# Kernel tuning notes

Hardware: AMD Instinct MI355X
Metric: run time of the kernel (lower is better)

Reference implementation:

```python
import jax, jax.numpy as jnp
import numpy as np
import math

# Model config (see init_kwargs)
E = 1024   # emb_size
H = 8      # ffwd_num_head
D = 128    # ffwd_head_size (E == H*D)
NE = 16    # ffwd_num_expert
A = 2      # ffwd_num_expert_active
S = 256    # ffwd_expert_size
B = 2      # batch_size_fwd
T = 2048   # context_window
NUM_BLOCK = 12


def setup_inputs() -> dict:
    key = jax.random.key(0)
    ks = jax.random.split(key, 5)
    x = jax.random.normal(ks[0], (B, T, E), jnp.float32)
    # fc_in_fused: Linear(E, 4E+NE, bias=False), torch weight shape (out,in)
    w_in = 0.02 * jax.random.normal(ks[1], (4 * E + NE, E), jnp.float32)
    # fc_out_fused: Linear(2E, E), std 0.02/sqrt(num_block)
    w_out = (0.02 / math.sqrt(NUM_BLOCK)) * jax.random.normal(ks[2], (E, 2 * E), jnp.float32)
    # k_ffwd/v_ffwd: original (1,H,NE*S,D); stored here as (NE,H,S,D) for per-expert scan
    k_ffwd = 0.02 * jax.random.normal(ks[3], (NE, H, S, D), jnp.float32)
    v_ffwd = 0.02 * jax.random.normal(ks[4], (NE, H, S, D), jnp.float32)
    return {"x": x, "w_in": w_in, "w_out": w_out, "k_ffwd": k_ffwd, "v_ffwd": v_ffwd}


def _rope(t):
    # Standard half-split RoPE, base 10000. t: (B,T,H,D)
    half = t.shape[-1] // 2
    inv_freq = 1.0 / (10000.0 ** (jnp.arange(half, dtype=jnp.float32) / half))
    ang = jnp.arange(t.shape[1], dtype=jnp.float32)[:, None] * inv_freq  # (T, half)
    cos = jnp.cos(ang)[None, :, None, :]
    sin = jnp.sin(ang)[None, :, None, :]
    t1, t2 = t[..., :half], t[..., half:]
    return jnp.concatenate([t1 * cos - t2 * sin, t1 * sin + t2 * cos], axis=-1)


def reference(x, w_in, w_out, k_ffwd, v_ffwd):
    Bx, Tx, _ = x.shape
    h = x @ w_in.T  # (B,T,4E+NE)
    q_f, q_a, k_a, v_a, router_logits = jnp.split(h, [E, 2 * E, 3 * E, 4 * E], axis=-1)

    # top-k routing (order of the k slots is irrelevant: outputs are summed)
    gate_logits, assign = jax.lax.top_k(router_logits, A)  # (B,T,A)
    gate = jax.nn.sigmoid(gate_logits)

    # --- attention half: causal softmax attention, scale 1/sqrt(D), with RoPE ---
    q = _rope(q_a.reshape(Bx, Tx, H, D))
    k = _rope(k_a.reshape(Bx, Tx, H, D))
    v = v_a.reshape(Bx, Tx, H, D)
    scores = jnp.einsum('bqhd,bkhd->bhqk', q, k) / math.sqrt(D)
    causal = jnp.tril(jnp.ones((Tx, Tx), dtype=bool))
    scores = jnp.where(causal, scores, -jnp.inf)
    p = jax.nn.softmax(scores, axis=-1)
    attn_out = jnp.einsum('bhqk,bkhd->bqhd', p, v).reshape(Bx, Tx, E)

    # --- MoE-FFN half, expressed as attention with score_mod log1p(gelu):
    # exp(lse)*softmax recovers sum_s (1+gelu(q.k_s)) v_s; subtracting sum_s v_s
    # leaves sum_s gelu(q.k_s) v_s over the assigned expert's slots. ---
    qf = q_f.reshape(Bx, Tx, H, D)

    def step(acc, ekv):
        e, ke, ve = ekv  # ke, ve: (H,S,D)
        s = jnp.einsum('bthd,hsd->bths', qf, ke)
        a = jax.nn.gelu(s, approximate=False)  # torch F.gelu default = exact erf
        o = jnp.einsum('bths,hsd->bthd', a, ve)
        g = jnp.sum(jnp.where(assign == e, gate, 0.0), axis=-1)  # (B,T)
        return acc + g[..., None, None] * o, None

    acc0 = jnp.zeros((Bx, Tx, H, D), x.dtype)
    ffwd_out, _ = jax.lax.scan(step, acc0, (jnp.arange(NE), k_ffwd, v_ffwd))
    ffwd_out = ffwd_out.reshape(Bx, Tx, E)

    out = jnp.concatenate([attn_out, ffwd_out], axis=-1) @ w_out.T  # (B,T,E)
    return out
```

## Files before the change

kernel.cpp:

```cpp
#include <hip/hip_runtime.h>
#include <hip/hip_bf16.h>
#include <math.h>

#define E 1024
#define NHP 4096
#define NEXP 16
#define HH 8
#define DD 128
#define SS 256
#define BB 2
#define TT 2048
#define BT 4096

typedef __attribute__((ext_vector_type(8))) short bf16x8;
typedef __attribute__((ext_vector_type(4))) float f32x4;

#define GLDS16(g, s) __builtin_amdgcn_global_load_lds( \
    (const __attribute__((address_space(1))) void*)(g), \
    (__attribute__((address_space(3))) void*)(s), 16, 0, 0)

__device__ __forceinline__ ushort f2b(float f) {
    union { float f; unsigned u; } v; v.f = f;
    unsigned r = (v.u + 0x7FFFu + ((v.u >> 16) & 1u)) >> 16;
    return (ushort)r;
}
__device__ __forceinline__ float b2f(ushort u) {
    union { unsigned u; float f; } v; v.u = ((unsigned)u) << 16;
    return v.f;
}
__device__ __forceinline__ float gelu_fast(float x) {
    float u2 = x * x;
    float tu = x * (1.5957691216f + 0.0713548163f * u2);
    float e = __expf(tu);
    float sig = 1.f - __builtin_amdgcn_rcpf(e + 1.f);
    return x * sig;
}

__global__ void cvtk_swz(const float* __restrict__ in, ushort* __restrict__ outp,
                         int kshift, int n)
{
    int i = (blockIdx.x * blockDim.x + threadIdx.x) * 8;
    if (i >= n) return;
    int row = i >> kshift;
    int colb = (i - (row << kshift)) * 2;
    float4 f0 = *(const float4*)(in + i);
    float4 f1 = *(const float4*)(in + i + 4);
    ushort4 u0, u1;
    u0.x = f2b(f0.x); u0.y = f2b(f0.y); u0.z = f2b(f0.z); u0.w = f2b(f0.w);
    u1.x = f2b(f1.x); u1.y = f2b(f1.y); u1.z = f2b(f1.z); u1.w = f2b(f1.w);
    char* dst = (char*)outp + ((size_t)row << (kshift + 1)) + (colb ^ ((row & 7) << 4));
    *(ushort4*)dst = u0;
    *(ushort4*)(dst + 8) = u1;
}

template<int BF16OUT>
__global__ __launch_bounds__(256) void gemm_bf16(
    const ushort* __restrict__ A, int lda,
    const ushort* __restrict__ B, int ldb,
    void* __restrict__ Cv, int ldc, int K)
{
    __shared__ ushort As[128 * 64];
    __shared__ ushort Bs[128 * 64];
    const int t = threadIdx.x;
    const int l = t & 63, w = t >> 6;
    const int m0 = blockIdx.y * 128, n0 = blockIdx.x * 128;
    const int wr = w >> 1, wc = w & 1;
    const int fr = l & 15, fg = l >> 4;

    const int srow = w * 32 + (l >> 3);
    const int sboff = (l & 7) * 16;
    const char* Ag = (const char*)A + ((size_t)(m0 + srow) * lda) * 2 + sboff;
    const char* Bg = (const char*)B + ((size_t)(n0 + srow) * ldb) * 2 + sboff;
    const int aswz = (fr & 7) << 4;

    f32x4 acc[4][4];
    #pragma unroll
    for (int i = 0; i < 4; ++i)
        #pragma unroll
        for (int j = 0; j < 4; ++j) { acc[i][j][0]=0.f; acc[i][j][1]=0.f; acc[i][j][2]=0.f; acc[i][j][3]=0.f; }

    for (int k0b = 0; k0b < K * 2; k0b += 128) {
        #pragma unroll
        for (int i = 0; i < 4; ++i) {
            GLDS16(Ag + (size_t)(i * 8) * lda * 2 + k0b, (char*)As + (w * 32 + i * 8) * 128);
            GLDS16(Bg + (size_t)(i * 8) * ldb * 2 + k0b, (char*)Bs + (w * 32 + i * 8) * 128);
        }
        __syncthreads();
        #pragma unroll
        for (int ksub = 0; ksub < 2; ++ksub) {
            bf16x8 a[4], b[4];
            #pragma unroll
            for (int mi = 0; mi < 4; ++mi)
                a[mi] = *(const bf16x8*)((const char*)As + (wr * 64 + mi * 16 + fr) * 128 + ((ksub * 64 + fg * 16) ^ aswz));
            #pragma unroll
            for (int ni = 0; ni < 4; ++ni)
                b[ni] = *(const bf16x8*)((const char*)Bs + (wc * 64 + ni * 16 + fr) * 128 + ((ksub * 64 + fg * 16) ^ aswz));
            #pragma unroll
            for (int mi = 0; mi < 4; ++mi)
                #pragma unroll
                for (int ni = 0; ni < 4; ++ni)
                    acc[mi][ni] = __builtin_amdgcn_mfma_f32_16x16x32_bf16(a[mi], b[ni], acc[mi][ni], 0, 0, 0);
        }
        __syncthreads();
    }
    #pragma unroll
    for (int mi = 0; mi < 4; ++mi)
        #pragma unroll
        for (int ni = 0; ni < 4; ++ni) {
            const int row = m0 + wr * 64 + mi * 16 + fg * 4;
            const int col = n0 + wc * 64 + ni * 16 + fr;
            #pragma unroll
            for (int r = 0; r < 4; ++r) {
                if (BF16OUT)
                    ((ushort*)Cv)[(size_t)(row + r) * ldc + col] = f2b(acc[mi][ni][r]);
                else
                    ((float*)Cv)[(size_t)(row + r) * ldc + col] = acc[mi][ni][r];
            }
        }
}

__global__ __launch_bounds__(256) void router_logits(
    const float* __restrict__ x, const float* __restrict__ w_in,
    float* __restrict__ gval, int* __restrict__ eidx)
{
    const int m = blockIdx.x * 4 + (threadIdx.x >> 6);
    const int lane = threadIdx.x & 63;

    const float* xp = x + (size_t)m * 1024 + lane * 4;
    float4 xv0 = *(const float4*)(xp);
    float4 xv1 = *(const float4*)(xp + 256);
    float4 xv2 = *(const float4*)(xp + 512);
    float4 xv3 = *(const float4*)(xp + 768);

    float p[16];
    #pragma unroll
    for (int e = 0; e < 16; ++e) {
        const float* wp = w_in + (size_t)(4096 + e) * 1024 + lane * 4;
        float4 w0 = *(const float4*)(wp);
        float4 w1 = *(const float4*)(wp + 256);
        float4 w2 = *(const float4*)(wp + 512);
        float4 w3 = *(const float4*)(wp + 768);
        float s0 = xv0.x * w0.x + xv0.y * w0.y + xv0.z * w0.z + xv0.w * w0.w;
        float s1 = xv1.x * w1.x + xv1.y * w1.y + xv1.z * w1.z + xv1.w * w1.w;
        float s2 = xv2.x * w2.x + xv2.y * w2.y + xv2.z * w2.z + xv2.w * w2.w;
        float s3 = xv3.x * w3.x + xv3.y * w3.y + xv3.z * w3.z + xv3.w * w3.w;
        p[e] = (s0 + s1) + (s2 + s3);
    }
    #pragma unroll
    for (int d = 1; d < 64; d <<= 1) {
        #pragma unroll
        for (int e = 0; e < 16; ++e)
            p[e] += __shfl_xor(p[e], d);
    }
    float best = -1e30f; int bi = 0;
    #pragma unroll
    for (int e = 0; e < 16; ++e)
        if (p[e] > best) { best = p[e]; bi = e; }
    float best2 = -1e30f; int bi2 = 0;
    #pragma unroll
    for (int e = 0; e < 16; ++e)
        if (e != bi && p[e] > best2) { best2 = p[e]; bi2 = e; }

    if (lane == 0) {
        gval[m * 2 + 0] = 1.f / (1.f + __expf(-best));
        gval[m * 2 + 1] = 1.f / (1.f + __expf(-best2));
        eidx[m * 2 + 0] = bi;
        eidx[m * 2 + 1] = bi2;
    }
}

__global__ __launch_bounds__(256) void build_lists(
    const int* __restrict__ eidx,
    int* __restrict__ counts, int* __restrict__ plist)
{
    const int e = blockIdx.x;
    const int t = threadIdx.x;
    const int w = t >> 6, lane = t & 63;
    __shared__ int wbase[4];
    __shared__ int running;
    if (t == 0) running = 0;
    __syncthreads();
    for (int c = 0; c < 2 * BT; c += 256) {
        const int p = c + t;
        const bool match = (eidx[p] == e);
        unsigned long long mask = __ballot(match);
        int lpre = __popcll(mask & ((lane == 63) ? 0x7FFFFFFFFFFFFFFFull
                                                 : ((1ull << lane) - 1ull)));
        if (lane == 0) wbase[w] = __popcll(mask);
        __syncthreads();
        int pre = running;
        #pragma unroll
        for (int i = 0; i < 4; ++i) if (i < w) pre += wbase[i];
        const int tot = wbase[0] + wbase[1] + wbase[2] + wbase[3];
        if (match) plist[e * BT + pre + lpre] = p;
        __syncthreads();
        if (t == 0) running += tot;
        __syncthreads();
    }
    if (t == 0) counts[e] = running;
}

__global__ void rope2(const ushort* __restrict__ hb,
                      ushort* __restrict__ qb, ushort* __restrict__ kb)
{
    int m = blockIdx.x;
    int t = threadIdx.x;
    int hd = t >> 6, j = t & 63;
    int tok = m & 2047, b = m >> 11;
    float invf = __expf(-(float)j * (9.210340371976184f / 64.f));
    float ang = (float)tok * invf;
    float s, c;
    sincosf(ang, &s, &c);
    const ushort* base = hb + (size_t)m * NHP + E + hd * DD;
    float q1 = b2f(base[j]), q2 = b2f(base[j + 64]);
    float k1 = b2f(base[E + j]), k2 = b2f(base[E + j + 64]);
    float qa = q1 * c - q2 * s, qbv = q1 * s + q2 * c;
    float ka = k1 * c - k2 * s, kbv = k1 * s + k2 * c;
    size_t rowb = ((size_t)(b * 8 + hd) * 2048 + tok) * 256;
    int sw = (tok & 7) << 4;
    *(ushort*)((char*)qb + rowb + ((2 * j) ^ sw))        = f2b(qa);
    *(ushort*)((char*)qb + rowb + ((2 * (j + 64)) ^ sw)) = f2b(qbv);
    *(ushort*)((char*)kb + rowb + ((2 * j) ^ sw))        = f2b(ka);
    *(ushort*)((char*)kb + rowb + ((2 * (j + 64)) ^ sw)) = f2b(kbv);
}

__global__ __launch_bounds__(256) void vtrans(const ushort* __restrict__ hb,
                                              ushort* __restrict__ vtb)
{
    __shared__ ushort T[64][132];
    int bh = blockIdx.y, ck = blockIdx.x;
    int b = bh >> 3, hd = bh & 7;
    int t = threadIdx.x;
    int tok0 = ck * 64;
    #pragma unroll
    for (int it = 0; it < 8; ++it) {
        int idx = it * 256 + t, r = idx >> 5, c4 = idx & 31;
        ushort4 f = *(const ushort4*)(hb + (size_t)(b * 2048 + tok0 + r) * NHP + 3 * E + hd * DD + c4 * 4);
        T[r][c4 * 4 + 0] = f.x; T[r][c4 * 4 + 1] = f.y;
        T[r][c4 * 4 + 2] = f.z; T[r][c4 * 4 + 3] = f.w;
    }
    __syncthreads();
    int g = t >> 4, fr = t & 15;
    #pragma unroll
    for (int dd = 0; dd < 8; ++dd) {
        int d = g + dd * 16;
        ushort4 u;
        u.x = T[4 * fr + 0][d]; u.y = T[4 * fr + 1][d];
        u.z = T[4 * fr + 2][d]; u.w = T[4 * fr + 3][d];
        size_t ob = ((size_t)(bh * 128 + d) * 2048 + tok0) * 2;
        *(ushort4*)((char*)vtb + ob + ((8 * fr) ^ ((d & 7) << 4))) = u;
    }
}

__global__ __launch_bounds__(256) void cvt_kv(
    const float* __restrict__ kf, const float* __restrict__ vf,
    ushort* __restrict__ kfb, ushort* __restrict__ vtf)
{
    __shared__ float T[64][132];
    int eh = blockIdx.y, st = blockIdx.x;
    int s0 = st * 64;
    int t = threadIdx.x;
    const float* kbp = kf + (size_t)eh * SS * DD + (size_t)s0 * DD;
    const float* vbp = vf + (size_t)eh * SS * DD + (size_t)s0 * DD;
    for (int i = t; i < 64 * 32; i += 256) {
        int r = i >> 5, c4 = i & 31;
        float4 f = *(const float4*)(kbp + (size_t)r * DD + c4 * 4);
        ushort4 u;
        u.x = f2b(f.x); u.y = f2b(f.y); u.z = f2b(f.z); u.w = f2b(f.w);
        *(ushort4*)((char*)kfb + ((size_t)eh * 256 + s0 + r) * 256 + ((c4 * 8) ^ ((r & 7) << 4))) = u;
    }
    for (int i = t; i < 64 * 32; i += 256) {
        int r = i >> 5, c4 = i & 31;
        float4 f = *(const float4*)(vbp + (size_t)r * DD + c4 * 4);
        T[r][c4 * 4 + 0] = f.x; T[r][c4 * 4 + 1] = f.y;
        T[r][c4 * 4 + 2] = f.z; T[r][c4 * 4 + 3] = f.w;
    }
    __syncthreads();
    int g = t >> 4, fr = t & 15;
    #pragma unroll
    for (int dd = 0; dd < 8; ++dd) {
        int d = g + dd * 16;
        ushort4 u;
        u.x = f2b(T[4 * fr + 0][d]); u.y = f2b(T[4 * fr + 1][d]);
        u.z = f2b(T[4 * fr + 2][d]); u.w = f2b(T[4 * fr + 3][d]);
        size_t ob = ((size_t)eh * 128 + d) * 512 + s0 * 2;
        *(ushort4*)((char*)vtf + ob + ((8 * fr) ^ ((d & 7) << 4))) = u;
    }
}

__global__ __launch_bounds__(512, 1) void attn_mfma(
    const ushort* __restrict__ qb, const ushort* __restrict__ kb,
    const ushort* __restrict__ vtb, ushort* __restrict__ catb)
{
    __shared__ ushort Ks[2][128 * 128];
    __shared__ ushort Vs[2][128 * 128];
    __shared__ ushort Ps[8][16 * 72];
    __shared__ float  LlS[8][16];

    const int t = threadIdx.x, l = t & 63, w = t >> 6;
    const int fr = l & 15, fg = l >> 4;
    const int wl = w & 3, hh = w >> 2;
    const int lin = blockIdx.x;
    const int bh = (lin & 7) * 2 + (lin >> 7);
    const int tpair = (lin >> 3) & 15;
    const int swz = (fr & 7) << 4;
    ushort* Pw = (ushort*)Ps[w];

    #pragma unroll 1
    for (int pass = 0; pass < 2; ++pass) {
        const int qt = pass ? (31 - tpair) : tpair;
        const int qbase = qt * 64;
        const int nkt = (qt + 2) >> 1;
        const int qg = qbase + wl * 16 + fg * 4;

        bf16x8 qreg[4];
        {
            const char* qrow = (const char*)qb + ((size_t)(bh * 2048 + qbase + wl * 16 + fr)) * 256;
            #pragma unroll
            for (int ks = 0; ks < 4; ++ks)
                qreg[ks] = *(const bf16x8*)(qrow + ((ks * 64 + fg * 16) ^ swz));
        }
        {
            const char* ksrc = (const char*)kb + ((size_t)(bh * 2048 + w * 16)) * 256;
            const char* vsrc = (const char*)vtb + ((size_t)(bh * 128 + w * 16)) * 4096;
            #pragma unroll
            for (int i = 0; i < 4; ++i) {
                GLDS16(ksrc + (size_t)(i * 4 + (l >> 4)) * 256 + (l & 15) * 16,
                       (char*)Ks[0] + (w * 16 + i * 4) * 256);
                GLDS16(vsrc + (size_t)(i * 4 + (l >> 4)) * 4096 + (l & 15) * 16,
                       (char*)Vs[0] + (w * 16 + i * 4) * 256);
            }
        }

        f32x4 po[8];
        #pragma unroll
        for (int i = 0; i < 8; ++i) { po[i][0]=0.f; po[i][1]=0.f; po[i][2]=0.f; po[i][3]=0.f; }
        float lrow[4] = {0.f, 0.f, 0.f, 0.f};

        asm volatile("s_waitcnt vmcnt(0)" ::: "memory");
        __syncthreads();

        for (int kt = 0; kt < nkt; ++kt) {
            const int cur = kt & 1;
            if (kt + 1 < nkt) {
                const int kvn = (kt + 1) * 128;
                const char* ksrc = (const char*)kb + ((size_t)(bh * 2048 + kvn + w * 16)) * 256;
                const char* vsrc = (const char*)vtb + ((size_t)(bh * 128 + w * 16)) * 4096 + kvn * 2;
                #pragma unroll
                for (int i = 0; i < 4; ++i) {
                    GLDS16(ksrc + (size_t)(i * 4 + (l >> 4)) * 256 + (l & 15) * 16,
                           (char*)Ks[cur ^ 1] + (w * 16 + i * 4) * 256);
                    GLDS16(vsrc + (size_t)(i * 4 + (l >> 4)) * 4096 + (l & 15) * 16,
                           (char*)Vs[cur ^ 1] + (w * 16 + i * 4) * 256);
                }
            }
            const int kvb = kt * 128;

            f32x4 s[4];
            #pragma unroll
            for (int i = 0; i < 4; ++i) { s[i][0]=0.f; s[i][1]=0.f; s[i][2]=0.f; s[i][3]=0.f; }
            __builtin_amdgcn_s_setprio(1);
            #pragma unroll
            for (int ks = 0; ks < 4; ++ks) {
                #pragma unroll
                for (int fn = 0; fn < 4; ++fn) {
                    const int brow = hh * 64 + fn * 16 + fr;
                    bf16x8 bb = *(const bf16x8*)((const char*)Ks[cur] + brow * 256 + ((ks * 64 + fg * 16) ^ swz));
                    s[fn] = __builtin_amdgcn_mfma_f32_16x16x32_bf16(qreg[ks], bb, s[fn], 0, 0, 0);
                }
            }
            __builtin_amdgcn_s_setprio(0);

            const int colbase = kvb + hh * 64;
            const bool needmask = (colbase + 64 > qbase + wl * 16);
            float ps[4] = {0.f, 0.f, 0.f, 0.f};
            #pragma unroll
            for (int fn = 0; fn < 4; ++fn)
                #pragma unroll
                for (int r = 0; r < 4; ++r) {
                    float v = s[fn][r] * 0.08838834764831845f;
                    bool masked = needmask && (colbase + fn * 16 + fr > qg + r);
                    float p = masked ? 0.f : __expf(v);
                    ps[r] += p;
                    Pw[(fg * 4 + r) * 72 + fn * 16 + fr] = f2b(p);
                }
            #pragma unroll
            for (int r = 0; r < 4; ++r) {
                float s2 = ps[r];
                s2 += __shfl_xor(s2, 1);
                s2 += __shfl_xor(s2, 2);
                s2 += __shfl_xor(s2, 4);
                s2 += __shfl_xor(s2, 8);
                lrow[r] += s2;
            }

            asm volatile("s_waitcnt lgkmcnt(0)" ::: "memory");
            __builtin_amdgcn_sched_barrier(0);

            __builtin_amdgcn_s_setprio(1);
            #pragma unroll
            for (int ks2 = 0; ks2 < 2; ++ks2) {
                bf16x8 pa = *(const bf16x8*)((const char*)Pw + fr * 144 + ks2 * 64 + fg * 16);
                #pragma unroll
                for (int fn2 = 0; fn2 < 8; ++fn2) {
                    const int vrow = fn2 * 16 + fr;
                    bf16x8 bv = *(const bf16x8*)((const char*)Vs[cur] + vrow * 256 + ((hh * 128 + ks2 * 64 + fg * 16) ^ swz));
                    po[fn2] = __builtin_amdgcn_mfma_f32_16x16x32_bf16(pa, bv, po[fn2], 0, 0, 0);
                }
            }
            __builtin_amdgcn_s_setprio(0);

            asm volatile("s_waitcnt vmcnt(0)" ::: "memory");
            __syncthreads();
        }

        if (fr == 0) {
            #pragma unroll
            for (int r = 0; r < 4; ++r)
                LlS[w][fg * 4 + r] = lrow[r];
        }
        __syncthreads();
        float linv[4];
        #pragma unroll
        for (int r = 0; r < 4; ++r)
            linv[r] = 1.f / (lrow[r] + LlS[w ^ 4][fg * 4 + r]);
        float* PO = (float*)&Ks[0][0];
        if (hh == 1) {
            #pragma unroll
            for (int fn2 = 0; fn2 < 8; ++fn2)
                #pragma unroll
                for (int r = 0; r < 4; ++r)
                    PO[(wl * 16 + fg * 4 + r) * 128 + fn2 * 16 + fr] = po[fn2][r];
        }
        __syncthreads();
        if (hh == 0) {
            const int mg = (bh >> 3) * 2048 + qbase + wl * 16 + fg * 4;
            #pragma unroll
            for (int r = 0; r < 4; ++r) {
                const int rswz = ((mg + r) & 7) << 4;
                #pragma unroll
                for (int fn2 = 0; fn2 < 8; ++fn2) {
                    float v = po[fn2][r] + PO[(wl * 16 + fg * 4 + r) * 128 + fn2 * 16 + fr];
                    int colb = ((bh & 7) * 128 + fn2 * 16 + fr) * 2;
                    *(ushort*)((char*)catb + (size_t)(mg + r) * 4096 + (colb ^ rswz)) = f2b(v * linv[r]);
                }
            }
        }
        __syncthreads();
    }
}

__global__ __launch_bounds__(256, 1) void ffn_mfma2(
    const ushort* __restrict__ hb,
    const float* __restrict__ gv,
    const int* __restrict__ counts,
    const int* __restrict__ plist,
    const ushort* __restrict__ kfb, const ushort* __restrict__ vtf,
    ushort* __restrict__ pairout)
{
    __shared__ ushort Ks[256 * 128];
    __shared__ ushort Vs[128 * 256];
    __shared__ ushort Qs[64 * 128];
    __shared__ ushort Ps[4][16 * 72];

    const int t = threadIdx.x, l = t & 63, w = t >> 6;
    const int fr = l & 15, fg = l >> 4;
    const int half = blockIdx.x, hd = blockIdx.y, e = blockIdx.z;
    const int eh = e * HH + hd;
    const int n_e = counts[e];

    {
        const char* kbase = (const char*)kfb + (size_t)eh * 65536;
        const char* vbase = (const char*)vtf + (size_t)eh * 65536;
        #pragma unroll
        for (int i = 0; i < 16; ++i) {
            GLDS16(kbase + (w * 64 + i * 4) * 256 + l * 16, (char*)Ks + (w * 64 + i * 4) * 256);
            GLDS16(vbase + w * 16384 + i * 1024 + l * 16, (char*)Vs + w * 16384 + i * 1024);
        }
    }
    __syncthreads();

    const int arow = w * 16 + fr;
    const int aswz = (arow & 7) << 4;
    ushort* Pw = (ushort*)Ps[w];
    const int rl4 = l >> 4;
    const int lb = (l & 15) * 16;

    for (int tb = half * 64; tb < n_e; tb += 128) {
        #pragma unroll
        for (int i = 0; i < 4; ++i) {
            int row = w * 16 + i * 4 + rl4;
            int gr = tb + row;
            int p = plist[e * BT + min(gr, n_e - 1)];
            int m = p >> 1;
            const char* src = (const char*)hb + (size_t)m * 8192 + hd * 256 + (lb ^ ((row & 7) << 4));
            GLDS16(src, (char*)Qs + (w * 16 + i * 4) * 256);
        }
        asm volatile("s_waitcnt vmcnt(0)" ::: "memory");

        f32x4 po[8];
        #pragma unroll
        for (int i = 0; i < 8; ++i) { po[i][0]=0.f; po[i][1]=0.f; po[i][2]=0.f; po[i][3]=0.f; }

        #pragma unroll
        for (int kt = 0; kt < 4; ++kt) {
            const int kvb = kt * 64;
            f32x4 s[4];
            #pragma unroll
            for (int i = 0; i < 4; ++i) { s[i][0]=0.f; s[i][1]=0.f; s[i][2]=0.f; s[i][3]=0.f; }
            #pragma unroll
            for (int ks = 0; ks < 4; ++ks) {
                bf16x8 a = *(const bf16x8*)((const char*)Qs + arow * 256 + ((ks * 64 + fg * 16) ^ aswz));
                #pragma unroll
                for (int fn = 0; fn < 4; ++fn) {
                    const int brow = kvb + fn * 16 + fr;
                    bf16x8 bb = *(const bf16x8*)((const char*)Ks + brow * 256 + ((ks * 64 + fg * 16) ^ ((brow & 7) << 4)));
                    s[fn] = __builtin_amdgcn_mfma_f32_16x16x32_bf16(a, bb, s[fn], 0, 0, 0);
                }
            }
            #pragma unroll
            for (int fn = 0; fn < 4; ++fn)
                #pragma unroll
                for (int r = 0; r < 4; ++r)
                    Pw[(fg * 4 + r) * 72 + fn * 16 + fr] = f2b(gelu_fast(s[fn][r]));
            asm volatile("s_waitcnt lgkmcnt(0)" ::: "memory");
            #pragma unroll
            for (int ks2 = 0; ks2 < 2; ++ks2) {
                bf16x8 pa = *(const bf16x8*)((const char*)Pw + fr * 144 + ks2 * 64 + fg * 16);
                #pragma unroll
                for (int fn2 = 0; fn2 < 8; ++fn2) {
                    const int vrow = fn2 * 16 + fr;
                    bf16x8 bv = *(const bf16x8*)((const char*)Vs + vrow * 512 + kt * 128 + ((ks2 * 64 + fg * 16) ^ ((vrow & 7) << 4)));
                    po[fn2] = __builtin_amdgcn_mfma_f32_16x16x32_bf16(pa, bv, po[fn2], 0, 0, 0);
                }
            }
        }
        const int rloc = w * 16 + fg * 4;
        #pragma unroll
        for (int r = 0; r < 4; ++r) {
            int gr = tb + rloc + r;
            if (gr < n_e) {
                int p = plist[e * BT + gr];
                float g = gv[p];
                #pragma unroll
                for (int fn2 = 0; fn2 < 8; ++fn2)
                    pairout[(size_t)p * 1024 + hd * DD + fn2 * 16 + fr] = f2b(g * po[fn2][r]);
            }
        }
    }
}

__global__ void combine_kernel(const ushort* __restrict__ po, ushort* __restrict__ catb)
{
    int i = blockIdx.x * blockDim.x + threadIdx.x;
    if (i >= BT * 128) return;
    int m = i >> 7, c = i & 127;
    const ushort* a = po + (size_t)(2 * m) * 1024 + c * 8;
    const ushort* b = po + (size_t)(2 * m + 1) * 1024 + c * 8;
    ushort4 a0 = *(const ushort4*)a, a1 = *(const ushort4*)(a + 4);
    ushort4 b0 = *(const ushort4*)b, b1 = *(const ushort4*)(b + 4);
    ushort4 o0, o1;
    o0.x = f2b(b2f(a0.x) + b2f(b0.x)); o0.y = f2b(b2f(a0.y) + b2f(b0.y));
    o0.z = f2b(b2f(a0.z) + b2f(b0.z)); o0.w = f2b(b2f(a0.w) + b2f(b0.w));
    o1.x = f2b(b2f(a1.x) + b2f(b1.x)); o1.y = f2b(b2f(a1.y) + b2f(b1.y));
    o1.z = f2b(b2f(a1.z) + b2f(b1.z)); o1.w = f2b(b2f(a1.w) + b2f(b1.w));
    char* dst = (char*)catb + (size_t)m * 4096 + 2048 + ((c * 16) ^ ((m & 7) << 4));
    *(ushort4*)dst = o0;
    *(ushort4*)(dst + 8) = o1;
}

extern "C" void kernel_launch(void* const* d_in, const int* in_sizes, int n_in,
                              void* d_out, int out_size, void* d_ws, size_t ws_size,
                              hipStream_t stream)
{
    const float* x     = (const float*)d_in[0];
    const float* w_in  = (const float*)d_in[1];
    const float* w_out = (const float*)d_in[2];
    const float* kf    = (const float*)d_in[3];
    const float* vf    = (const float*)d_in[4];
    float* out = (float*)d_out;

    char* W = (char*)d_ws;
    ushort* hb      = (ushort*)(W + 0);
    ushort* xb      = (ushort*)(W + 33554432);
    ushort* wib     = (ushort*)(W + 41943040);
    ushort* kfb     = xb;
    ushort* vtf     = wib;
    ushort* wob     = (ushort*)(W + 50331648);
    ushort* qb2     = (ushort*)(W + 54525952);
    ushort* kb2     = (ushort*)(W + 62914560);
    ushort* vtb     = (ushort*)(W + 71303168);
    ushort* catb    = (ushort*)(W + 79691776);
    ushort* pairout = (ushort*)(W + 96468992);
    float*  gv      = (float*)(W + 113246208);
    int*    counts  = (int*)(W + 113278976);
    int*    plist   = (int*)(W + 113279040);
    int*    eidx    = (int*)(W + 113541184);

    cvtk_swz<<<2048, 256, 0, stream>>>(x, xb, 10, 4096 * 1024);
    cvtk_swz<<<2048, 256, 0, stream>>>(w_in, wib, 10, 4096 * 1024);
    cvtk_swz<<<1024, 256, 0, stream>>>(w_out, wob, 11, 1024 * 2048);

    router_logits<<<BT / 4, 256, 0, stream>>>(x, w_in, gv, eidx);
    build_lists<<<NEXP, 256, 0, stream>>>(eidx, counts, plist);

    gemm_bf16<1><<<dim3(32, 32), 256, 0, stream>>>(xb, 1024, wib, 1024, hb, NHP, 1024);

    rope2<<<BT, 512, 0, stream>>>(hb, qb2, kb2);
    vtrans<<<dim3(32, 16), 256, 0, stream>>>(hb, vtb);
    cvt_kv<<<dim3(4, NEXP * HH), 256, 0, stream>>>(kf, vf, kfb, vtf);

    attn_mfma<<<dim3(256), 512, 0, stream>>>(qb2, kb2, vtb, catb);

    ffn_mfma2<<<dim3(2, HH, NEXP), 256, 0, stream>>>(hb, gv, counts, plist, kfb, vtf, pairout);
    combine_kernel<<<2048, 256, 0, stream>>>(pairout, catb);

    gemm_bf16<0><<<dim3(8, 32), 256, 0, stream>>>(catb, 2048, wob, 2048, out, 1024, 2048);
}
```

Baseline: 243.6 us.

## Fuse x bf16 conversion into router; restructure attention to one q-tile per block

The router kernel now writes the swizzled bf16 copy of x while it already holds x in registers, which removes a separate conversion launch and a second read of x. The attention kernel changes from 256 blocks of 512 threads, each handling two paired q-tiles and splitting the key range across two wave halves, to 512 blocks of 256 threads that each handle one q-tile over 64-wide key tiles. This drops the cross-wave reduction through shared memory and the extra syncs, and lowers shared memory use so more blocks can fit per CU. In exchange each block runs more loop iterations with smaller tiles, and load balance now depends on the block scheduler instead of the explicit tile pairing.

```diff
diff --git a/kernel.cpp b/kernel.cpp
--- a/kernel.cpp
+++ b/kernel.cpp
@@ -121,7 +121,7 @@
 
 __global__ __launch_bounds__(256) void router_logits(
     const float* __restrict__ x, const float* __restrict__ w_in,
-    float* __restrict__ gval, int* __restrict__ eidx)
+    float* __restrict__ gval, int* __restrict__ eidx, ushort* __restrict__ xb)
 {
     const int m = blockIdx.x * 4 + (threadIdx.x >> 6);
     const int lane = threadIdx.x & 63;
@@ -131,6 +131,20 @@
     float4 xv1 = *(const float4*)(xp + 256);
     float4 xv2 = *(const float4*)(xp + 512);
     float4 xv3 = *(const float4*)(xp + 768);
+
+    {
+        const int swrow = (m & 7) << 4;
+        char* xrow = (char*)xb + (size_t)m * 2048;
+        ushort4 u;
+        u.x = f2b(xv0.x); u.y = f2b(xv0.y); u.z = f2b(xv0.z); u.w = f2b(xv0.w);
+        *(ushort4*)(xrow + ((lane * 8 + 0 * 512) ^ swrow)) = u;
+        u.x = f2b(xv1.x); u.y = f2b(xv1.y); u.z = f2b(xv1.z); u.w = f2b(xv1.w);
+        *(ushort4*)(xrow + ((lane * 8 + 1 * 512) ^ swrow)) = u;
+        u.x = f2b(xv2.x); u.y = f2b(xv2.y); u.z = f2b(xv2.z); u.w = f2b(xv2.w);
+        *(ushort4*)(xrow + ((lane * 8 + 2 * 512) ^ swrow)) = u;
+        u.x = f2b(xv3.x); u.y = f2b(xv3.y); u.z = f2b(xv3.z); u.w = f2b(xv3.w);
+        *(ushort4*)(xrow + ((lane * 8 + 3 * 512) ^ swrow)) = u;
+    }
 
     float p[16];
     #pragma unroll
@@ -288,165 +302,138 @@
     }
 }
 
-__global__ __launch_bounds__(512, 1) void attn_mfma(
+__global__ __launch_bounds__(256) void attn_mfma(
     const ushort* __restrict__ qb, const ushort* __restrict__ kb,
     const ushort* __restrict__ vtb, ushort* __restrict__ catb)
 {
-    __shared__ ushort Ks[2][128 * 128];
-    __shared__ ushort Vs[2][128 * 128];
-    __shared__ ushort Ps[8][16 * 72];
-    __shared__ float  LlS[8][16];
+    __shared__ ushort Ks[2][64 * 128];
+    __shared__ ushort Vs[2][128 * 64];
+    __shared__ ushort Ps[4][16 * 72];
 
     const int t = threadIdx.x, l = t & 63, w = t >> 6;
     const int fr = l & 15, fg = l >> 4;
-    const int wl = w & 3, hh = w >> 2;
     const int lin = blockIdx.x;
-    const int bh = (lin & 7) * 2 + (lin >> 7);
-    const int tpair = (lin >> 3) & 15;
+    const int a = lin & 255, s = lin >> 8;
+    const int xcd = a & 7, idx = a >> 3;
+    const int bh = xcd * 2 + (idx & 1);
+    const int q5 = idx >> 1;
+    const int qt = s ? (31 - q5) : q5;
+    const int qbase = qt * 64;
+    const int nkt = qt + 1;
     const int swz = (fr & 7) << 4;
     ushort* Pw = (ushort*)Ps[w];
-
-    #pragma unroll 1
-    for (int pass = 0; pass < 2; ++pass) {
-        const int qt = pass ? (31 - tpair) : tpair;
-        const int qbase = qt * 64;
-        const int nkt = (qt + 2) >> 1;
-        const int qg = qbase + wl * 16 + fg * 4;
-
-        bf16x8 qreg[4];
-        {
-            const char* qrow = (const char*)qb + ((size_t)(bh * 2048 + qbase + wl * 16 + fr)) * 256;
-            #pragma unroll
-            for (int ks = 0; ks < 4; ++ks)
-                qreg[ks] = *(const bf16x8*)(qrow + ((ks * 64 + fg * 16) ^ swz));
-        }
-        {
-            const char* ksrc = (const char*)kb + ((size_t)(bh * 2048 + w * 16)) * 256;
-            const char* vsrc = (const char*)vtb + ((size_t)(bh * 128 + w * 16)) * 4096;
+    const int qg = qbase + w * 16 + fg * 4;
+
+    bf16x8 qreg[4];
+    {
+        const char* qrow = (const char*)qb + ((size_t)(bh * 2048 + qbase + w * 16 + fr)) * 256;
+        #pragma unroll
+        for (int ks = 0; ks < 4; ++ks)
+            qreg[ks] = *(const bf16x8*)(qrow + ((ks * 64 + fg * 16) ^ swz));
+    }
+    {
+        const char* ksrc = (const char*)kb + ((size_t)(bh * 2048)) * 256;
+        const char* vsrc = (const char*)vtb + ((size_t)(bh * 128 + w * 32)) * 4096;
+        #pragma unroll
+        for (int i = 0; i < 4; ++i) {
+            GLDS16(ksrc + (size_t)(w * 16 + i * 4 + (l >> 4)) * 256 + (l & 15) * 16,
+                   (char*)Ks[0] + (w * 16 + i * 4) * 256);
+            GLDS16(vsrc + (size_t)(i * 8 + (l >> 3)) * 4096 + (l & 7) * 16,
+                   (char*)Vs[0] + (w * 32 + i * 8) * 128);
+        }
+    }
+
+    f32x4 po[8];
+    #pragma unroll
+    for (int i = 0; i < 8; ++i) { po[i][0]=0.f; po[i][1]=0.f; po[i][2]=0.f; po[i][3]=0.f; }
+    float lrow[4] = {0.f, 0.f, 0.f, 0.f};
+
+    asm volatile("s_waitcnt vmcnt(0)" ::: "memory");
+    __syncthreads();
+
+    for (int kt = 0; kt < nkt; ++kt) {
+        const int cur = kt & 1;
+        if (kt + 1 < nkt) {
+            const int kvn = (kt + 1) * 64;
+            const char* ksrc = (const char*)kb + ((size_t)(bh * 2048 + kvn)) * 256;
+            const char* vsrc = (const char*)vtb + ((size_t)(bh * 128 + w * 32)) * 4096 + kvn * 2;
             #pragma unroll
             for (int i = 0; i < 4; ++i) {
-                GLDS16(ksrc + (size_t)(i * 4 + (l >> 4)) * 256 + (l & 15) * 16,
-                       (char*)Ks[0] + (w * 16 + i * 4) * 256);
-                GLDS16(vsrc + (size_t)(i * 4 + (l >> 4)) * 4096 + (l & 15) * 16,
-                       (char*)Vs[0] + (w * 16 + i * 4) * 256);
-            }
-        }
-
-        f32x4 po[8];
-        #pragma unroll
-        for (int i = 0; i < 8; ++i) { po[i][0]=0.f; po[i][1]=0.f; po[i][2]=0.f; po[i][3]=0.f; }
-        float lrow[4] = {0.f, 0.f, 0.f, 0.f};
+                GLDS16(ksrc + (size_t)(w * 16 + i * 4 + (l >> 4)) * 256 + (l & 15) * 16,
+                       (char*)Ks[cur ^ 1] + (w * 16 + i * 4) * 256);
+                GLDS16(vsrc + (size_t)(i * 8 + (l >> 3)) * 4096 + (l & 7) * 16,
+                       (char*)Vs[cur ^ 1] + (w * 32 + i * 8) * 128);
+            }
+        }
+        const int kvb = kt * 64;
+
+        f32x4 sA[4];
+        #pragma unroll
+        for (int i = 0; i < 4; ++i) { sA[i][0]=0.f; sA[i][1]=0.f; sA[i][2]=0.f; sA[i][3]=0.f; }
+        __builtin_amdgcn_s_setprio(1);
+        #pragma unroll
+        for (int ks = 0; ks < 4; ++ks) {
+            #pragma unroll
+            for (int fn = 0; fn < 4; ++fn) {
+                const int brow = fn * 16 + fr;
+                bf16x8 bb = *(const bf16x8*)((const char*)Ks[cur] + brow * 256 + ((ks * 64 + fg * 16) ^ swz));
+                sA[fn] = __builtin_amdgcn_mfma_f32_16x16x32_bf16(qreg[ks], bb, sA[fn], 0, 0, 0);
+            }
+        }
+        __builtin_amdgcn_s_setprio(0);
+
+        const bool diag = (kvb == qbase);
+        float ps[4] = {0.f, 0.f, 0.f, 0.f};
+        #pragma unroll
+        for (int fn = 0; fn < 4; ++fn)
+            #pragma unroll
+            for (int r = 0; r < 4; ++r) {
+                float v = sA[fn][r] * 0.08838834764831845f;
+                bool masked = diag && (kvb + fn * 16 + fr > qg + r);
+                float p = masked ? 0.f : __expf(v);
+                ps[r] += p;
+                Pw[(fg * 4 + r) * 72 + fn * 16 + fr] = f2b(p);
+            }
+        #pragma unroll
+        for (int r = 0; r < 4; ++r) {
+            float s2 = ps[r];
+            s2 += __shfl_xor(s2, 1);
+            s2 += __shfl_xor(s2, 2);
+            s2 += __shfl_xor(s2, 4);
+            s2 += __shfl_xor(s2, 8);
+            lrow[r] += s2;
+        }
+
+        asm volatile("s_waitcnt lgkmcnt(0)" ::: "memory");
+        __builtin_amdgcn_sched_barrier(0);
+
+        __builtin_amdgcn_s_setprio(1);
+        #pragma unroll
+        for (int ks2 = 0; ks2 < 2; ++ks2) {
+            bf16x8 pa = *(const bf16x8*)((const char*)Pw + fr * 144 + ks2 * 64 + fg * 16);
+            #pragma unroll
+            for (int fn2 = 0; fn2 < 8; ++fn2) {
+                const int vrow = fn2 * 16 + fr;
+                bf16x8 bv = *(const bf16x8*)((const char*)Vs[cur] + vrow * 128 + ((ks2 * 64 + fg * 16) ^ swz));
+                po[fn2] = __builtin_amdgcn_mfma_f32_16x16x32_bf16(pa, bv, po[fn2], 0, 0, 0);
+            }
+        }
+        __builtin_amdgcn_s_setprio(0);
 
         asm volatile("s_waitcnt vmcnt(0)" ::: "memory");
         __syncthreads();
-
-        for (int kt = 0; kt < nkt; ++kt) {
-            const int cur = kt & 1;
-            if (kt + 1 < nkt) {
-                const int kvn = (kt + 1) * 128;
-                const char* ksrc = (const char*)kb + ((size_t)(bh * 2048 + kvn + w * 16)) * 256;
-                const char* vsrc = (const char*)vtb + ((size_t)(bh * 128 + w * 16)) * 4096 + kvn * 2;
-                #pragma unroll
-                for (int i = 0; i < 4; ++i) {
-                    GLDS16(ksrc + (size_t)(i * 4 + (l >> 4)) * 256 + (l & 15) * 16,
-                           (char*)Ks[cur ^ 1] + (w * 16 + i * 4) * 256);
-                    GLDS16(vsrc + (size_t)(i * 4 + (l >> 4)) * 4096 + (l & 15) * 16,
-                           (char*)Vs[cur ^ 1] + (w * 16 + i * 4) * 256);
-                }
-            }
-            const int kvb = kt * 128;
-
-            f32x4 s[4];
-            #pragma unroll
-            for (int i = 0; i < 4; ++i) { s[i][0]=0.f; s[i][1]=0.f; s[i][2]=0.f; s[i][3]=0.f; }
-            __builtin_amdgcn_s_setprio(1);
-            #pragma unroll
-            for (int ks = 0; ks < 4; ++ks) {
-                #pragma unroll
-                for (int fn = 0; fn < 4; ++fn) {
-                    const int brow = hh * 64 + fn * 16 + fr;
-                    bf16x8 bb = *(const bf16x8*)((const char*)Ks[cur] + brow * 256 + ((ks * 64 + fg * 16) ^ swz));
-                    s[fn] = __builtin_amdgcn_mfma_f32_16x16x32_bf16(qreg[ks], bb, s[fn], 0, 0, 0);
-                }
-            }
-            __builtin_amdgcn_s_setprio(0);
-
-            const int colbase = kvb + hh * 64;
-            const bool needmask = (colbase + 64 > qbase + wl * 16);
-            float ps[4] = {0.f, 0.f, 0.f, 0.f};
-            #pragma unroll
-            for (int fn = 0; fn < 4; ++fn)
-                #pragma unroll
-                for (int r = 0; r < 4; ++r) {
-                    float v = s[fn][r] * 0.08838834764831845f;
-                    bool masked = needmask && (colbase + fn * 16 + fr > qg + r);
-                    float p = masked ? 0.f : __expf(v);
-                    ps[r] += p;
-                    Pw[(fg * 4 + r) * 72 + fn * 16 + fr] = f2b(p);
-                }
-            #pragma unroll
-            for (int r = 0; r < 4; ++r) {
-                float s2 = ps[r];
-                s2 += __shfl_xor(s2, 1);
-                s2 += __shfl_xor(s2, 2);
-                s2 += __shfl_xor(s2, 4);
-                s2 += __shfl_xor(s2, 8);
-                lrow[r] += s2;
-            }
-
-            asm volatile("s_waitcnt lgkmcnt(0)" ::: "memory");
-            __builtin_amdgcn_sched_barrier(0);
-
-            __builtin_amdgcn_s_setprio(1);
-            #pragma unroll
-            for (int ks2 = 0; ks2 < 2; ++ks2) {
-                bf16x8 pa = *(const bf16x8*)((const char*)Pw + fr * 144 + ks2 * 64 + fg * 16);
-                #pragma unroll
-                for (int fn2 = 0; fn2 < 8; ++fn2) {
-                    const int vrow = fn2 * 16 + fr;
-                    bf16x8 bv = *(const bf16x8*)((const char*)Vs[cur] + vrow * 256 + ((hh * 128 + ks2 * 64 + fg * 16) ^ swz));
-                    po[fn2] = __builtin_amdgcn_mfma_f32_16x16x32_bf16(pa, bv, po[fn2], 0, 0, 0);
-                }
-            }
-            __builtin_amdgcn_s_setprio(0);
-
-            asm volatile("s_waitcnt vmcnt(0)" ::: "memory");
-            __syncthreads();
-        }
-
-        if (fr == 0) {
-            #pragma unroll
-            for (int r = 0; r < 4; ++r)
-                LlS[w][fg * 4 + r] = lrow[r];
-        }
-        __syncthreads();
-        float linv[4];
-        #pragma unroll
-        for (int r = 0; r < 4; ++r)
-            linv[r] = 1.f / (lrow[r] + LlS[w ^ 4][fg * 4 + r]);
-        float* PO = (float*)&Ks[0][0];
-        if (hh == 1) {
-            #pragma unroll
-            for (int fn2 = 0; fn2 < 8; ++fn2)
-                #pragma unroll
-                for (int r = 0; r < 4; ++r)
-                    PO[(wl * 16 + fg * 4 + r) * 128 + fn2 * 16 + fr] = po[fn2][r];
-        }
-        __syncthreads();
-        if (hh == 0) {
-            const int mg = (bh >> 3) * 2048 + qbase + wl * 16 + fg * 4;
-            #pragma unroll
-            for (int r = 0; r < 4; ++r) {
-                const int rswz = ((mg + r) & 7) << 4;
-                #pragma unroll
-                for (int fn2 = 0; fn2 < 8; ++fn2) {
-                    float v = po[fn2][r] + PO[(wl * 16 + fg * 4 + r) * 128 + fn2 * 16 + fr];
-                    int colb = ((bh & 7) * 128 + fn2 * 16 + fr) * 2;
-                    *(ushort*)((char*)catb + (size_t)(mg + r) * 4096 + (colb ^ rswz)) = f2b(v * linv[r]);
-                }
-            }
-        }
-        __syncthreads();
+    }
+
+    const int mg = (bh >> 3) * 2048 + qbase + w * 16 + fg * 4;
+    #pragma unroll
+    for (int r = 0; r < 4; ++r) {
+        float linv = 1.f / lrow[r];
+        const int rswz = ((mg + r) & 7) << 4;
+        #pragma unroll
+        for (int fn2 = 0; fn2 < 8; ++fn2) {
+            int colb = ((bh & 7) * 128 + fn2 * 16 + fr) * 2;
+            *(ushort*)((char*)catb + (size_t)(mg + r) * 4096 + (colb ^ rswz)) = f2b(po[fn2][r] * linv);
+        }
     }
 }
 
@@ -505,24 +492,24 @@
         #pragma unroll
         for (int kt = 0; kt < 4; ++kt) {
             const int kvb = kt * 64;
-            f32x4 s[4];
-            #pragma unroll
-            for (int i = 0; i < 4; ++i) { s[i][0]=0.f; s[i][1]=0.f; s[i][2]=0.f; s[i][3]=0.f; }
+            f32x4 sA[4];
+            #pragma unroll
+            for (int i = 0; i < 4; ++i) { sA[i][0]=0.f; sA[i][1]=0.f; sA[i][2]=0.f; sA[i][3]=0.f; }
             #pragma unroll
             for (int ks = 0; ks < 4; ++ks) {
-                bf16x8 a = *(const bf16x8*)((const char*)Qs + arow * 256 + ((ks * 64 + fg * 16) ^ aswz));
+                bf16x8 aa = *(const bf16x8*)((const char*)Qs + arow * 256 + ((ks * 64 + fg * 16) ^ aswz));
                 #pragma unroll
                 for (int fn = 0; fn < 4; ++fn) {
                     const int brow = kvb + fn * 16 + fr;
                     bf16x8 bb = *(const bf16x8*)((const char*)Ks + brow * 256 + ((ks * 64 + fg * 16) ^ ((brow & 7) << 4)));
-                    s[fn] = __builtin_amdgcn_mfma_f32_16x16x32_bf16(a, bb, s[fn], 0, 0, 0);
+                    sA[fn] = __builtin_amdgcn_mfma_f32_16x16x32_bf16(aa, bb, sA[fn], 0, 0, 0);
                 }
             }
             #pragma unroll
             for (int fn = 0; fn < 4; ++fn)
                 #pragma unroll
                 for (int r = 0; r < 4; ++r)
-                    Pw[(fg * 4 + r) * 72 + fn * 16 + fr] = f2b(gelu_fast(s[fn][r]));
+                    Pw[(fg * 4 + r) * 72 + fn * 16 + fr] = f2b(gelu_fast(sA[fn][r]));
             asm volatile("s_waitcnt lgkmcnt(0)" ::: "memory");
             #pragma unroll
             for (int ks2 = 0; ks2 < 2; ++ks2) {
@@ -597,11 +584,10 @@
     int*    plist   = (int*)(W + 113279040);
     int*    eidx    = (int*)(W + 113541184);
 
-    cvtk_swz<<<2048, 256, 0, stream>>>(x, xb, 10, 4096 * 1024);
     cvtk_swz<<<2048, 256, 0, stream>>>(w_in, wib, 10, 4096 * 1024);
     cvtk_swz<<<1024, 256, 0, stream>>>(w_out, wob, 11, 1024 * 2048);
 
-    router_logits<<<BT / 4, 256, 0, stream>>>(x, w_in, gv, eidx);
+    router_logits<<<BT / 4, 256, 0, stream>>>(x, w_in, gv, eidx, xb);
     build_lists<<<NEXP, 256, 0, stream>>>(eidx, counts, plist);
 
     gemm_bf16<1><<<dim3(32, 32), 256, 0, stream>>>(xb, 1024, wib, 1024, hb, NHP, 1024);
@@ -610,7 +596,7 @@
     vtrans<<<dim3(32, 16), 256, 0, stream>>>(hb, vtb);
     cvt_kv<<<dim3(4, NEXP * HH), 256, 0, stream>>>(kf, vf, kfb, vtf);
 
-    attn_mfma<<<dim3(256), 512, 0, stream>>>(qb2, kb2, vtb, catb);
+    attn_mfma<<<dim3(512), 256, 0, stream>>>(qb2, kb2, vtb, catb);
 
     ffn_mfma2<<<dim3(2, HH, NEXP), 256, 0, stream>>>(hb, gv, counts, plist, kfb, vtf, pairout);
     combine_kernel<<<2048, 256, 0, stream>>>(pairout, catb);
```

Measured after the change: 256.1 us. 1.05x slower.
